# Kernel optimization log

Measured on AMD Instinct MI355X. Metric: run time of the kernel, lower is better.

The kernel has to match this reference:

```python
import jax, jax.numpy as jnp
import numpy as np

WORLD_SIZE = 8
BS = 16
MSG = 16384


def setup_inputs() -> dict:
    key = jax.random.key(0)
    k0, k1, kw, kb = jax.random.split(key, 4)
    x0 = jax.random.normal(k0, (WORLD_SIZE, BS, MSG), dtype=jnp.float32)
    x1 = jax.random.normal(k1, (WORLD_SIZE, BS, MSG), dtype=jnp.float32)
    # nn.Linear(msg_size, msg_size) params, kaiming-uniform-ish scale
    scale = 1.0 / np.sqrt(MSG)
    W = jax.random.uniform(kw, (MSG, MSG), dtype=jnp.float32, minval=-scale, maxval=scale)
    b = jax.random.uniform(kb, (MSG,), dtype=jnp.float32, minval=-scale, maxval=scale)
    return {"x0": x0, "x1": x1, "W": W, "b": b}


def reference(x0, x1, W, b):
    # all_gather_ll: concat per-rank shards along dim 0 -> [world_size*bs, msg]
    t0 = x0.reshape(WORLD_SIZE * BS, MSG)
    t1 = x1.reshape(WORLD_SIZE * BS, MSG)
    # shared Linear applied to both gathered tensors: y = t @ W^T + b
    y0 = jnp.einsum("nk,mk->nm", t0, W) + b
    y1 = jnp.einsum("nk,mk->nm", t1, W) + b
    return (y0, y1)
```

## Files before the change

### kernel.cpp

```cpp
#include <hip/hip_runtime.h>
#include <hip/hip_bf16.h>

typedef __bf16 bf16x8 __attribute__((ext_vector_type(8)));
typedef float  f32x4  __attribute__((ext_vector_type(4)));

#define N_TOT   16384
#define K_TOT   16384
#define HALF_M  ((size_t)128 * 16384)
#define BN      128
#define BK      64
#define KSPLIT  4
#define KQ_LEN  (K_TOT / KSPLIT)
#define NQSTEPS (KQ_LEN / BK)
#define OUT_ELEMS ((size_t)256 * 16384)

__device__ __forceinline__ unsigned short f2bf(float f) {
    __hip_bfloat16 h = __float2bfloat16(f);
    return __builtin_bit_cast(unsigned short, h);
}

__device__ __forceinline__ int swz(int row, int g) {
    return row * 128 + (((g ^ (row & 7)) & 7) << 4);
}

__global__ void cvtT_kernel(const float* __restrict__ x0,
                            const float* __restrict__ x1,
                            unsigned short* __restrict__ wsT) {
    size_t i = (size_t)blockIdx.x * blockDim.x + threadIdx.x;
    size_t e = i * 8;
    const float* src = (e < HALF_M) ? (x0 + e) : (x1 + (e - HALF_M));
    float4 a = ((const float4*)src)[0];
    float4 b = ((const float4*)src)[1];
    union { unsigned short u[8]; uint4 v; } o;
    o.u[0] = f2bf(a.x); o.u[1] = f2bf(a.y); o.u[2] = f2bf(a.z); o.u[3] = f2bf(a.w);
    o.u[4] = f2bf(b.x); o.u[5] = f2bf(b.y); o.u[6] = f2bf(b.z); o.u[7] = f2bf(b.w);
    ((uint4*)wsT)[i] = o.v;
}

__global__ void combine_kernel(float* __restrict__ out,
                               const float* __restrict__ p0,
                               const float* __restrict__ p1,
                               const float* __restrict__ p2) {
    const size_t n4 = OUT_ELEMS / 4;
    size_t i = (size_t)blockIdx.x * blockDim.x + threadIdx.x;
    for (; i < n4; i += (size_t)gridDim.x * blockDim.x) {
        float4 o = ((const float4*)out)[i];
        float4 a = ((const float4*)p0)[i];
        float4 b = ((const float4*)p1)[i];
        float4 c = ((const float4*)p2)[i];
        o.x += a.x + b.x + c.x;  o.y += a.y + b.y + c.y;
        o.z += a.z + b.z + c.z;  o.w += a.w + b.w + c.w;
        ((float4*)out)[i] = o;
    }
}

#define ISSUEW(S, k0) do {                                                    \
    const uint4* _p = (const uint4*)(arow_w + (k0));                          \
    w##S##_0 = _p[0]; w##S##_1 = _p[1];                                       \
    const float4* _q = (const float4*)(brow + (k0));                          \
    wb##S##_0 = _q[0]; wb##S##_1 = _q[1];                                     \
} while (0)

#define STAGEW(S, Ab, Bb) do {                                                \
    *(uint4*)((Ab) + aw0) = w##S##_0;                                         \
    *(uint4*)((Ab) + aw1) = w##S##_1;                                         \
    union { unsigned short u[8]; uint4 v; } _tb;                              \
    _tb.u[0]=f2bf(wb##S##_0.x); _tb.u[1]=f2bf(wb##S##_0.y);                   \
    _tb.u[2]=f2bf(wb##S##_0.z); _tb.u[3]=f2bf(wb##S##_0.w);                   \
    _tb.u[4]=f2bf(wb##S##_1.x); _tb.u[5]=f2bf(wb##S##_1.y);                   \
    _tb.u[6]=f2bf(wb##S##_1.z); _tb.u[7]=f2bf(wb##S##_1.w);                   \
    *(uint4*)((Bb) + bw) = _tb.v;                                             \
} while (0)

#define COMPUTE(Ab, Bb) do {                                                  \
    bf16x8 _b00 = *(const bf16x8*)((Bb) + boff00);                            \
    bf16x8 _b01 = *(const bf16x8*)((Bb) + boff01);                            \
    bf16x8 _b10 = *(const bf16x8*)((Bb) + boff10);                            \
    bf16x8 _b11 = *(const bf16x8*)((Bb) + boff11);                            \
    bf16x8 _a;                                                                \
    _a = *(const bf16x8*)((Ab) + aoff00);                                     \
    acc00 = __builtin_amdgcn_mfma_f32_16x16x32_bf16(_a, _b00, acc00, 0, 0, 0);\
    acc01 = __builtin_amdgcn_mfma_f32_16x16x32_bf16(_a, _b10, acc01, 0, 0, 0);\
    _a = *(const bf16x8*)((Ab) + aoff01);                                     \
    acc00 = __builtin_amdgcn_mfma_f32_16x16x32_bf16(_a, _b01, acc00, 0, 0, 0);\
    acc01 = __builtin_amdgcn_mfma_f32_16x16x32_bf16(_a, _b11, acc01, 0, 0, 0);\
    _a = *(const bf16x8*)((Ab) + aoff10);                                     \
    acc10 = __builtin_amdgcn_mfma_f32_16x16x32_bf16(_a, _b00, acc10, 0, 0, 0);\
    acc11 = __builtin_amdgcn_mfma_f32_16x16x32_bf16(_a, _b10, acc11, 0, 0, 0);\
    _a = *(const bf16x8*)((Ab) + aoff11);                                     \
    acc10 = __builtin_amdgcn_mfma_f32_16x16x32_bf16(_a, _b01, acc10, 0, 0, 0);\
    acc11 = __builtin_amdgcn_mfma_f32_16x16x32_bf16(_a, _b11, acc11, 0, 0, 0);\
    _a = *(const bf16x8*)((Ab) + aoff20);                                     \
    acc20 = __builtin_amdgcn_mfma_f32_16x16x32_bf16(_a, _b00, acc20, 0, 0, 0);\
    acc21 = __builtin_amdgcn_mfma_f32_16x16x32_bf16(_a, _b10, acc21, 0, 0, 0);\
    _a = *(const bf16x8*)((Ab) + aoff21);                                     \
    acc20 = __builtin_amdgcn_mfma_f32_16x16x32_bf16(_a, _b01, acc20, 0, 0, 0);\
    acc21 = __builtin_amdgcn_mfma_f32_16x16x32_bf16(_a, _b11, acc21, 0, 0, 0);\
    _a = *(const bf16x8*)((Ab) + aoff30);                                     \
    acc30 = __builtin_amdgcn_mfma_f32_16x16x32_bf16(_a, _b00, acc30, 0, 0, 0);\
    acc31 = __builtin_amdgcn_mfma_f32_16x16x32_bf16(_a, _b10, acc31, 0, 0, 0);\
    _a = *(const bf16x8*)((Ab) + aoff31);                                     \
    acc30 = __builtin_amdgcn_mfma_f32_16x16x32_bf16(_a, _b01, acc30, 0, 0, 0);\
    acc31 = __builtin_amdgcn_mfma_f32_16x16x32_bf16(_a, _b11, acc31, 0, 0, 0);\
} while (0)

#define SYNC do {                                                             \
    asm volatile("s_waitcnt lgkmcnt(0)" ::: "memory");                        \
    __builtin_amdgcn_s_barrier();                                             \
    __builtin_amdgcn_sched_barrier(0);                                        \
} while (0)

__global__ __launch_bounds__(1024, 4)
void gemm_ws(const float* __restrict__ W, const float* __restrict__ bias,
             const unsigned short* __restrict__ wsT,
             float* __restrict__ out, float* __restrict__ wsP)
{
    __shared__ uint4 smem_[(2 * 32768 + 2 * 16384) / 16];
    char* const sm = (char*)smem_;
    char* const A0 = sm;
    char* const A1 = sm + 32768;
    char* const B0 = sm + 65536;
    char* const B1 = sm + 65536 + 16384;

    const int tid  = threadIdx.x;
    const int lane = tid & 63;
    const int wave = tid >> 6;
    const int wm = wave >> 2;
    const int wn = wave & 3;
    const int bid    = blockIdx.x;
    const int kq     = (bid & 7) >> 1;
    const int nstrip = ((bid >> 3) << 1) + (bid & 1);
    const int n0     = nstrip * BN;
    const int kbase  = kq * KQ_LEN;

    const int ra  = tid >> 2;
    const int pa  = tid & 3;
    const int rbs = tid >> 3;

    const unsigned short* arow_w = wsT + (size_t)ra * K_TOT + kbase + pa * 16;
    const float* brow = W + (size_t)(n0 + rbs) * K_TOT + kbase + (tid & 7) * 8;

    const int aw0 = swz(ra, 2 * pa);
    const int aw1 = swz(ra, 2 * pa + 1);
    const int bw  = swz(rbs, tid & 7);

    const int aoff00 = swz(wm * 64 +  0 + (lane & 15), 0 + (lane >> 4));
    const int aoff01 = swz(wm * 64 +  0 + (lane & 15), 4 + (lane >> 4));
    const int aoff10 = swz(wm * 64 + 16 + (lane & 15), 0 + (lane >> 4));
    const int aoff11 = swz(wm * 64 + 16 + (lane & 15), 4 + (lane >> 4));
    const int aoff20 = swz(wm * 64 + 32 + (lane & 15), 0 + (lane >> 4));
    const int aoff21 = swz(wm * 64 + 32 + (lane & 15), 4 + (lane >> 4));
    const int aoff30 = swz(wm * 64 + 48 + (lane & 15), 0 + (lane >> 4));
    const int aoff31 = swz(wm * 64 + 48 + (lane & 15), 4 + (lane >> 4));
    const int boff00 = swz(wn * 32 +  0 + (lane & 15), 0 + (lane >> 4));
    const int boff01 = swz(wn * 32 +  0 + (lane & 15), 4 + (lane >> 4));
    const int boff10 = swz(wn * 32 + 16 + (lane & 15), 0 + (lane >> 4));
    const int boff11 = swz(wn * 32 + 16 + (lane & 15), 4 + (lane >> 4));

    f32x4 acc00 = {0.f,0.f,0.f,0.f}, acc01 = {0.f,0.f,0.f,0.f};
    f32x4 acc10 = {0.f,0.f,0.f,0.f}, acc11 = {0.f,0.f,0.f,0.f};
    f32x4 acc20 = {0.f,0.f,0.f,0.f}, acc21 = {0.f,0.f,0.f,0.f};
    f32x4 acc30 = {0.f,0.f,0.f,0.f}, acc31 = {0.f,0.f,0.f,0.f};

    uint4  w0_0, w0_1, w1_0, w1_1;
    float4 wb0_0, wb0_1, wb1_0, wb1_1;

    ISSUEW(0, 0);
    ISSUEW(1, BK);
    STAGEW(0, A0, B0);
    SYNC;

    for (int kt = 0; kt < NQSTEPS; kt += 2) {
        if (kt + 2 < NQSTEPS) ISSUEW(0, (kt + 2) * BK);
        COMPUTE(A0, B0);
        STAGEW(1, A1, B1);
        SYNC;
        if (kt + 3 < NQSTEPS) ISSUEW(1, (kt + 3) * BK);
        COMPUTE(A1, B1);
        if (kt + 2 < NQSTEPS) STAGEW(0, A0, B0);
        SYNC;
    }

    float* const dst = (kq == 0) ? out : (wsP + (size_t)(kq - 1) * OUT_ELEMS);
    #pragma unroll
    for (int nf = 0; nf < 2; ++nf) {
        const int col = n0 + wn * 32 + nf * 16 + (lane & 15);
        const float bv = (kq == 0) ? bias[col] : 0.f;
        #pragma unroll
        for (int mf = 0; mf < 4; ++mf) {
            const f32x4 a =
                (nf == 0) ? (mf == 0 ? acc00 : mf == 1 ? acc10 : mf == 2 ? acc20 : acc30)
                          : (mf == 0 ? acc01 : mf == 1 ? acc11 : mf == 2 ? acc21 : acc31);
            #pragma unroll
            for (int j = 0; j < 4; ++j) {
                int r = wm * 64 + mf * 16 + (lane >> 4) * 4 + j;
                float v = a[j] + bv;
                float* o = (r < 128) ? (dst + (size_t)r * N_TOT + col)
                                     : (dst + HALF_M + (size_t)(r - 128) * N_TOT + col);
                *o = v;
            }
        }
    }
}

extern "C" void kernel_launch(void* const* d_in, const int* in_sizes, int n_in,
                              void* d_out, int out_size, void* d_ws, size_t ws_size,
                              hipStream_t stream) {
    const float* x0 = (const float*)d_in[0];
    const float* x1 = (const float*)d_in[1];
    const float* W  = (const float*)d_in[2];
    const float* b  = (const float*)d_in[3];
    float* out = (float*)d_out;

    const size_t wsT_bytes = (size_t)256 * 16384 * sizeof(unsigned short);

    unsigned short* wsT = (unsigned short*)d_ws;
    float* wsP = (float*)((char*)d_ws + wsT_bytes);

    cvtT_kernel<<<2048, 256, 0, stream>>>(x0, x1, wsT);
    gemm_ws<<<512, 1024, 0, stream>>>(W, b, wsT, out, wsP);
    combine_kernel<<<2048, 256, 0, stream>>>(out, wsP, wsP + OUT_ELEMS,
                                             wsP + 2 * OUT_ELEMS);
}
```

Measured before the change: 317.9 us.

## Halve GEMM block to 512 threads with BK=32 and larger per-wave M tile

The GEMM block drops from 1024 to 512 threads and BK from 64 to 32, which halves LDS use per block. Each wave now covers 128 rows by 32 columns with 16 accumulators instead of 8, and the LDS swizzle is reworked for 64-byte rows. The block-to-(kq, nstrip) mapping becomes linear, changing which blocks share W strips at the same time. The aim is more A-fragment reuse per B load and better occupancy from the smaller LDS footprint, at the cost of twice as many barriers per K range and more register pressure.

```diff
diff --git a/kernel.cpp b/kernel.cpp
--- a/kernel.cpp
+++ b/kernel.cpp
@@ -8,7 +8,7 @@
 #define K_TOT   16384
 #define HALF_M  ((size_t)128 * 16384)
 #define BN      128
-#define BK      64
+#define BK      32
 #define KSPLIT  4
 #define KQ_LEN  (K_TOT / KSPLIT)
 #define NQSTEPS (KQ_LEN / BK)
@@ -19,8 +19,8 @@
     return __builtin_bit_cast(unsigned short, h);
 }
 
-__device__ __forceinline__ int swz(int row, int g) {
-    return row * 128 + (((g ^ (row & 7)) & 7) << 4);
+__device__ __forceinline__ int swz64(int row, int g) {
+    return row * 64 + (((g ^ ((row >> 1) & 3)) & 3) << 4);
 }
 
 __global__ void cvtT_kernel(const float* __restrict__ x0,
@@ -73,35 +73,33 @@
 } while (0)
 
 #define COMPUTE(Ab, Bb) do {                                                  \
-    bf16x8 _b00 = *(const bf16x8*)((Bb) + boff00);                            \
-    bf16x8 _b01 = *(const bf16x8*)((Bb) + boff01);                            \
-    bf16x8 _b10 = *(const bf16x8*)((Bb) + boff10);                            \
-    bf16x8 _b11 = *(const bf16x8*)((Bb) + boff11);                            \
-    bf16x8 _a;                                                                \
-    _a = *(const bf16x8*)((Ab) + aoff00);                                     \
-    acc00 = __builtin_amdgcn_mfma_f32_16x16x32_bf16(_a, _b00, acc00, 0, 0, 0);\
-    acc01 = __builtin_amdgcn_mfma_f32_16x16x32_bf16(_a, _b10, acc01, 0, 0, 0);\
-    _a = *(const bf16x8*)((Ab) + aoff01);                                     \
-    acc00 = __builtin_amdgcn_mfma_f32_16x16x32_bf16(_a, _b01, acc00, 0, 0, 0);\
-    acc01 = __builtin_amdgcn_mfma_f32_16x16x32_bf16(_a, _b11, acc01, 0, 0, 0);\
-    _a = *(const bf16x8*)((Ab) + aoff10);                                     \
-    acc10 = __builtin_amdgcn_mfma_f32_16x16x32_bf16(_a, _b00, acc10, 0, 0, 0);\
-    acc11 = __builtin_amdgcn_mfma_f32_16x16x32_bf16(_a, _b10, acc11, 0, 0, 0);\
-    _a = *(const bf16x8*)((Ab) + aoff11);                                     \
-    acc10 = __builtin_amdgcn_mfma_f32_16x16x32_bf16(_a, _b01, acc10, 0, 0, 0);\
-    acc11 = __builtin_amdgcn_mfma_f32_16x16x32_bf16(_a, _b11, acc11, 0, 0, 0);\
-    _a = *(const bf16x8*)((Ab) + aoff20);                                     \
-    acc20 = __builtin_amdgcn_mfma_f32_16x16x32_bf16(_a, _b00, acc20, 0, 0, 0);\
-    acc21 = __builtin_amdgcn_mfma_f32_16x16x32_bf16(_a, _b10, acc21, 0, 0, 0);\
-    _a = *(const bf16x8*)((Ab) + aoff21);                                     \
-    acc20 = __builtin_amdgcn_mfma_f32_16x16x32_bf16(_a, _b01, acc20, 0, 0, 0);\
-    acc21 = __builtin_amdgcn_mfma_f32_16x16x32_bf16(_a, _b11, acc21, 0, 0, 0);\
-    _a = *(const bf16x8*)((Ab) + aoff30);                                     \
-    acc30 = __builtin_amdgcn_mfma_f32_16x16x32_bf16(_a, _b00, acc30, 0, 0, 0);\
-    acc31 = __builtin_amdgcn_mfma_f32_16x16x32_bf16(_a, _b10, acc31, 0, 0, 0);\
-    _a = *(const bf16x8*)((Ab) + aoff31);                                     \
-    acc30 = __builtin_amdgcn_mfma_f32_16x16x32_bf16(_a, _b01, acc30, 0, 0, 0);\
-    acc31 = __builtin_amdgcn_mfma_f32_16x16x32_bf16(_a, _b11, acc31, 0, 0, 0);\
+    bf16x8 _vb0 = *(const bf16x8*)((Bb) + boff0);                             \
+    bf16x8 _vb1 = *(const bf16x8*)((Bb) + boff0 + 1024);                      \
+    bf16x8 _va;                                                               \
+    _va = *(const bf16x8*)((Ab) + aoff0 + 0*1024);                            \
+    accA0 = __builtin_amdgcn_mfma_f32_16x16x32_bf16(_va, _vb0, accA0, 0,0,0); \
+    accB0 = __builtin_amdgcn_mfma_f32_16x16x32_bf16(_va, _vb1, accB0, 0,0,0); \
+    _va = *(const bf16x8*)((Ab) + aoff0 + 1*1024);                            \
+    accA1 = __builtin_amdgcn_mfma_f32_16x16x32_bf16(_va, _vb0, accA1, 0,0,0); \
+    accB1 = __builtin_amdgcn_mfma_f32_16x16x32_bf16(_va, _vb1, accB1, 0,0,0); \
+    _va = *(const bf16x8*)((Ab) + aoff0 + 2*1024);                            \
+    accA2 = __builtin_amdgcn_mfma_f32_16x16x32_bf16(_va, _vb0, accA2, 0,0,0); \
+    accB2 = __builtin_amdgcn_mfma_f32_16x16x32_bf16(_va, _vb1, accB2, 0,0,0); \
+    _va = *(const bf16x8*)((Ab) + aoff0 + 3*1024);                            \
+    accA3 = __builtin_amdgcn_mfma_f32_16x16x32_bf16(_va, _vb0, accA3, 0,0,0); \
+    accB3 = __builtin_amdgcn_mfma_f32_16x16x32_bf16(_va, _vb1, accB3, 0,0,0); \
+    _va = *(const bf16x8*)((Ab) + aoff0 + 4*1024);                            \
+    accA4 = __builtin_amdgcn_mfma_f32_16x16x32_bf16(_va, _vb0, accA4, 0,0,0); \
+    accB4 = __builtin_amdgcn_mfma_f32_16x16x32_bf16(_va, _vb1, accB4, 0,0,0); \
+    _va = *(const bf16x8*)((Ab) + aoff0 + 5*1024);                            \
+    accA5 = __builtin_amdgcn_mfma_f32_16x16x32_bf16(_va, _vb0, accA5, 0,0,0); \
+    accB5 = __builtin_amdgcn_mfma_f32_16x16x32_bf16(_va, _vb1, accB5, 0,0,0); \
+    _va = *(const bf16x8*)((Ab) + aoff0 + 6*1024);                            \
+    accA6 = __builtin_amdgcn_mfma_f32_16x16x32_bf16(_va, _vb0, accA6, 0,0,0); \
+    accB6 = __builtin_amdgcn_mfma_f32_16x16x32_bf16(_va, _vb1, accB6, 0,0,0); \
+    _va = *(const bf16x8*)((Ab) + aoff0 + 7*1024);                            \
+    accA7 = __builtin_amdgcn_mfma_f32_16x16x32_bf16(_va, _vb0, accA7, 0,0,0); \
+    accB7 = __builtin_amdgcn_mfma_f32_16x16x32_bf16(_va, _vb1, accB7, 0,0,0); \
 } while (0)
 
 #define SYNC do {                                                             \
@@ -110,17 +108,17 @@
     __builtin_amdgcn_sched_barrier(0);                                        \
 } while (0)
 
-__global__ __launch_bounds__(1024, 4)
+__global__ __launch_bounds__(512, 4)
 void gemm_ws(const float* __restrict__ W, const float* __restrict__ bias,
              const unsigned short* __restrict__ wsT,
              float* __restrict__ out, float* __restrict__ wsP)
 {
-    __shared__ uint4 smem_[(2 * 32768 + 2 * 16384) / 16];
+    __shared__ uint4 smem_[(2 * 16384 + 2 * 8192) / 16];
     char* const sm = (char*)smem_;
     char* const A0 = sm;
-    char* const A1 = sm + 32768;
-    char* const B0 = sm + 65536;
-    char* const B1 = sm + 65536 + 16384;
+    char* const A1 = sm + 16384;
+    char* const B0 = sm + 32768;
+    char* const B1 = sm + 32768 + 8192;
 
     const int tid  = threadIdx.x;
     const int lane = tid & 63;
@@ -128,39 +126,34 @@
     const int wm = wave >> 2;
     const int wn = wave & 3;
     const int bid    = blockIdx.x;
-    const int kq     = (bid & 7) >> 1;
-    const int nstrip = ((bid >> 3) << 1) + (bid & 1);
+    const int kq     = bid >> 7;
+    const int nstrip = bid & 127;
     const int n0     = nstrip * BN;
     const int kbase  = kq * KQ_LEN;
 
-    const int ra  = tid >> 2;
-    const int pa  = tid & 3;
-    const int rbs = tid >> 3;
+    const int ra = tid >> 1;
+    const int pa = tid & 1;
+    const int rb = tid >> 2;
+    const int gb = tid & 3;
 
     const unsigned short* arow_w = wsT + (size_t)ra * K_TOT + kbase + pa * 16;
-    const float* brow = W + (size_t)(n0 + rbs) * K_TOT + kbase + (tid & 7) * 8;
-
-    const int aw0 = swz(ra, 2 * pa);
-    const int aw1 = swz(ra, 2 * pa + 1);
-    const int bw  = swz(rbs, tid & 7);
-
-    const int aoff00 = swz(wm * 64 +  0 + (lane & 15), 0 + (lane >> 4));
-    const int aoff01 = swz(wm * 64 +  0 + (lane & 15), 4 + (lane >> 4));
-    const int aoff10 = swz(wm * 64 + 16 + (lane & 15), 0 + (lane >> 4));
-    const int aoff11 = swz(wm * 64 + 16 + (lane & 15), 4 + (lane >> 4));
-    const int aoff20 = swz(wm * 64 + 32 + (lane & 15), 0 + (lane >> 4));
-    const int aoff21 = swz(wm * 64 + 32 + (lane & 15), 4 + (lane >> 4));
-    const int aoff30 = swz(wm * 64 + 48 + (lane & 15), 0 + (lane >> 4));
-    const int aoff31 = swz(wm * 64 + 48 + (lane & 15), 4 + (lane >> 4));
-    const int boff00 = swz(wn * 32 +  0 + (lane & 15), 0 + (lane >> 4));
-    const int boff01 = swz(wn * 32 +  0 + (lane & 15), 4 + (lane >> 4));
-    const int boff10 = swz(wn * 32 + 16 + (lane & 15), 0 + (lane >> 4));
-    const int boff11 = swz(wn * 32 + 16 + (lane & 15), 4 + (lane >> 4));
-
-    f32x4 acc00 = {0.f,0.f,0.f,0.f}, acc01 = {0.f,0.f,0.f,0.f};
-    f32x4 acc10 = {0.f,0.f,0.f,0.f}, acc11 = {0.f,0.f,0.f,0.f};
-    f32x4 acc20 = {0.f,0.f,0.f,0.f}, acc21 = {0.f,0.f,0.f,0.f};
-    f32x4 acc30 = {0.f,0.f,0.f,0.f}, acc31 = {0.f,0.f,0.f,0.f};
+    const float* brow = W + (size_t)(n0 + rb) * K_TOT + kbase + gb * 8;
+
+    const int aw0 = swz64(ra, 2 * pa);
+    const int aw1 = swz64(ra, 2 * pa + 1);
+    const int bw  = swz64(rb, gb);
+
+    const int aoff0 = swz64(wm * 128 + (lane & 15), lane >> 4);
+    const int boff0 = swz64(wn * 32 + (lane & 15), lane >> 4);
+
+    f32x4 accA0={0.f,0.f,0.f,0.f}, accA1={0.f,0.f,0.f,0.f};
+    f32x4 accA2={0.f,0.f,0.f,0.f}, accA3={0.f,0.f,0.f,0.f};
+    f32x4 accA4={0.f,0.f,0.f,0.f}, accA5={0.f,0.f,0.f,0.f};
+    f32x4 accA6={0.f,0.f,0.f,0.f}, accA7={0.f,0.f,0.f,0.f};
+    f32x4 accB0={0.f,0.f,0.f,0.f}, accB1={0.f,0.f,0.f,0.f};
+    f32x4 accB2={0.f,0.f,0.f,0.f}, accB3={0.f,0.f,0.f,0.f};
+    f32x4 accB4={0.f,0.f,0.f,0.f}, accB5={0.f,0.f,0.f,0.f};
+    f32x4 accB6={0.f,0.f,0.f,0.f}, accB7={0.f,0.f,0.f,0.f};
 
     uint4  w0_0, w0_1, w1_0, w1_1;
     float4 wb0_0, wb0_1, wb1_0, wb1_1;
@@ -187,13 +180,15 @@
         const int col = n0 + wn * 32 + nf * 16 + (lane & 15);
         const float bv = (kq == 0) ? bias[col] : 0.f;
         #pragma unroll
-        for (int mf = 0; mf < 4; ++mf) {
-            const f32x4 a =
-                (nf == 0) ? (mf == 0 ? acc00 : mf == 1 ? acc10 : mf == 2 ? acc20 : acc30)
-                          : (mf == 0 ? acc01 : mf == 1 ? acc11 : mf == 2 ? acc21 : acc31);
+        for (int mf = 0; mf < 8; ++mf) {
+            const f32x4 a = (nf == 0)
+                ? (mf==0?accA0:mf==1?accA1:mf==2?accA2:mf==3?accA3:
+                   mf==4?accA4:mf==5?accA5:mf==6?accA6:accA7)
+                : (mf==0?accB0:mf==1?accB1:mf==2?accB2:mf==3?accB3:
+                   mf==4?accB4:mf==5?accB5:mf==6?accB6:accB7);
             #pragma unroll
             for (int j = 0; j < 4; ++j) {
-                int r = wm * 64 + mf * 16 + (lane >> 4) * 4 + j;
+                int r = wm * 128 + mf * 16 + (lane >> 4) * 4 + j;
                 float v = a[j] + bv;
                 float* o = (r < 128) ? (dst + (size_t)r * N_TOT + col)
                                      : (dst + HALF_M + (size_t)(r - 128) * N_TOT + col);
@@ -218,7 +213,7 @@
     float* wsP = (float*)((char*)d_ws + wsT_bytes);
 
     cvtT_kernel<<<2048, 256, 0, stream>>>(x0, x1, wsT);
-    gemm_ws<<<512, 1024, 0, stream>>>(W, b, wsT, out, wsP);
+    gemm_ws<<<512, 512, 0, stream>>>(W, b, wsT, out, wsP);
     combine_kernel<<<2048, 256, 0, stream>>>(out, wsP, wsP + OUT_ELEMS,
                                              wsP + 2 * OUT_ELEMS);
 }
```

Result: no change. 322.6 us (+1.5%).
